# Kernel optimization log

Measured on AMD Instinct MI355X. Metric: run time of the kernel, lower is better.

The kernel has to match this reference:

```python
import math
import jax, jax.numpy as jnp
import numpy as np

DIM = 256
B, S = 4, 4096

def setup_inputs() -> dict:
    key = jax.random.key(0)
    k1, k2, k3 = jax.random.split(key, 3)
    X = jax.random.normal(k1, (B, S, DIM), dtype=jnp.float32)
    # torch nn.Linear(dim, 3*dim): weight [3*dim, dim], bias [3*dim]
    bound = 1.0 / math.sqrt(DIM)
    W = jax.random.uniform(k2, (3 * DIM, DIM), minval=-bound, maxval=bound, dtype=jnp.float32)
    b = jax.random.uniform(k3, (3 * DIM,), minval=-bound, maxval=bound, dtype=jnp.float32)
    return {"X": X, "W": W, "b": b}

def reference(X, W, b):
    # fused QKV projection: X @ W^T + b -> [B, S, 3*dim]
    QKV = jnp.einsum('bsd,ed->bse', X, W) + b
    Q, K, V = jnp.split(QKV, 3, axis=-1)
    # scaled dot-product attention (naive, full score matrix per original)
    scores = jnp.einsum('bqd,bkd->bqk', Q, K) / math.sqrt(DIM)
    att = jax.nn.softmax(scores, axis=-1)
    return jnp.einsum('bqk,bkd->bqd', att, V)
```

## Files before the change

### kernel.cpp

```cpp
#include <hip/hip_runtime.h>
#include <hip/hip_bf16.h>

#define B_ 4
#define S_ 4096
#define D_ 256

typedef __attribute__((ext_vector_type(8))) short bf16x8;
typedef __attribute__((ext_vector_type(4))) short short4v;
typedef __attribute__((ext_vector_type(4))) float f32x4;

static __device__ __forceinline__ unsigned short f2bf(float f) {
    unsigned int u = __float_as_uint(f);
    u += 0x7fffu + ((u >> 16) & 1u);
    return (unsigned short)(u >> 16);
}
static __device__ __forceinline__ float bf2f(unsigned short h) {
    return __uint_as_float(((unsigned int)h) << 16);
}
static __device__ __forceinline__ unsigned int cvtpk(float lo, float hi) {
    unsigned int r;
    asm("v_cvt_pk_bf16_f32 %0, %1, %2" : "=v"(r) : "v"(lo), "v"(hi));
    return r;
}

static __device__ __forceinline__ void gload16(const void* g, void* l) {
    __builtin_amdgcn_global_load_lds(
        (const __attribute__((address_space(1))) unsigned int*)g,
        (__attribute__((address_space(3))) unsigned int*)l, 16, 0, 0);
}

__global__ __launch_bounds__(256) void qkv_proj(
    const float* __restrict__ X, const float* __restrict__ W,
    const float* __restrict__ bias,
    unsigned short* __restrict__ Qb, unsigned short* __restrict__ Kb,
    unsigned short* __restrict__ Vt)
{
    __shared__ __align__(16) unsigned short As[64 * 64];
    __shared__ __align__(16) unsigned short Bs[64 * 64];

    const int tid  = threadIdx.x;
    const int lane = tid & 63;
    const int wid  = tid >> 6;
    const int wm   = wid >> 1, wn = wid & 1;
    const int c    = lane & 15, q4 = lane >> 4;
    const int gm0  = blockIdx.x * 64;
    const int gn0  = blockIdx.y * 64;
    const int sr   = tid >> 2;
    const int sc   = (tid & 3) * 16;

    f32x4 acc[2][2] = {};

    for (int kt = 0; kt < 4; ++kt) {
        const int k0 = kt * 64;
        {
            const float4* ga = (const float4*)(X + (size_t)(gm0 + sr) * D_ + k0 + sc);
            const float4* gb = (const float4*)(W + (size_t)(gn0 + sr) * D_ + k0 + sc);
            float4 a0 = ga[0], a1 = ga[1], a2 = ga[2], a3 = ga[3];
            float4 b0 = gb[0], b1 = gb[1], b2 = gb[2], b3 = gb[3];
            float af[16] = {a0.x,a0.y,a0.z,a0.w, a1.x,a1.y,a1.z,a1.w,
                            a2.x,a2.y,a2.z,a2.w, a3.x,a3.y,a3.z,a3.w};
            float bf[16] = {b0.x,b0.y,b0.z,b0.w, b1.x,b1.y,b1.z,b1.w,
                            b2.x,b2.y,b2.z,b2.w, b3.x,b3.y,b3.z,b3.w};
            bf16x8 av0, av1, bv0, bv1;
            #pragma unroll
            for (int j = 0; j < 8; ++j) {
                av0[j] = (short)f2bf(af[j]);     av1[j] = (short)f2bf(af[8 + j]);
                bv0[j] = (short)f2bf(bf[j]);     bv1[j] = (short)f2bf(bf[8 + j]);
            }
            const int sw = (sr & 7) << 3;
            *(bf16x8*)&As[sr * 64 + ((sc + 0) ^ sw)] = av0;
            *(bf16x8*)&As[sr * 64 + ((sc + 8) ^ sw)] = av1;
            *(bf16x8*)&Bs[sr * 64 + ((sc + 0) ^ sw)] = bv0;
            *(bf16x8*)&Bs[sr * 64 + ((sc + 8) ^ sw)] = bv1;
        }
        __syncthreads();
        const int sw = (c & 7) << 3;
        #pragma unroll
        for (int kk = 0; kk < 64; kk += 32) {
            bf16x8 afr[2], bfr[2];
            #pragma unroll
            for (int mf = 0; mf < 2; ++mf) {
                const int row = wm * 32 + mf * 16 + c;
                afr[mf] = *(const bf16x8*)&As[row * 64 + ((kk + 8 * q4) ^ sw)];
            }
            #pragma unroll
            for (int nf = 0; nf < 2; ++nf) {
                const int row = wn * 32 + nf * 16 + c;
                bfr[nf] = *(const bf16x8*)&Bs[row * 64 + ((kk + 8 * q4) ^ sw)];
            }
            #pragma unroll
            for (int mf = 0; mf < 2; ++mf)
                #pragma unroll
                for (int nf = 0; nf < 2; ++nf)
                    acc[mf][nf] = __builtin_amdgcn_mfma_f32_16x16x32_bf16(
                        afr[mf], bfr[nf], acc[mf][nf], 0, 0, 0);
        }
        __syncthreads();
    }

    const int b  = gm0 >> 12;
    const int s0 = gm0 & 4095;
    #pragma unroll
    for (int mf = 0; mf < 2; ++mf) {
        #pragma unroll
        for (int nf = 0; nf < 2; ++nf) {
            const int e  = gn0 + wn * 32 + nf * 16 + c;
            const float bv = bias[e];
            const int srow0 = s0 + wm * 32 + mf * 16 + 4 * q4;
            if (e < 256) {
                #pragma unroll
                for (int i = 0; i < 4; ++i)
                    Qb[((size_t)b * S_ + srow0 + i) * D_ + e] =
                        f2bf(acc[mf][nf][i] + bv);
            } else if (e < 512) {
                #pragma unroll
                for (int i = 0; i < 4; ++i)
                    Kb[((size_t)b * S_ + srow0 + i) * D_ + (e - 256)] =
                        f2bf(acc[mf][nf][i] + bv);
            } else {
                short4v pv;
                #pragma unroll
                for (int i = 0; i < 4; ++i)
                    pv[i] = (short)f2bf(acc[mf][nf][i] + bv);
                *(short4v*)&Vt[((size_t)(b * D_ + (e - 512))) * S_ + srow0] = pv;
            }
        }
    }
}

__global__ __launch_bounds__(512, 2) void attn_fwd(
    const unsigned short* __restrict__ Qb, const unsigned short* __restrict__ Kb,
    const unsigned short* __restrict__ Vt, float* __restrict__ Out)
{
    __shared__ __align__(16) char smem[132096];

    const int bid  = blockIdx.x;
    const int xcd  = bid & 7;
    const int tile = (xcd >> 1) * 64 + (bid >> 3) * 2 + (xcd & 1);
    const int gr0  = tile * 64;
    const int b    = gr0 >> 12;

    const int tid  = threadIdx.x;
    const int wid  = tid >> 6, lane = tid & 63;
    const int qi   = lane & 15, g = lane >> 4;
    const int rg   = wid & 3;
    const int kh   = wid >> 2;
    const int q0   = gr0 + rg * 16;
    const float C  = 0.09016844005556021f;
    const float THR = 40.0f;

    bf16x8 qf[8];
    {
        const size_t qrow = (size_t)(q0 + qi) * D_ + 8 * g;
        #pragma unroll
        for (int m = 0; m < 8; ++m)
            qf[m] = *(const bf16x8*)&Qb[qrow + m * 32];
    }

    const unsigned short* Kbb = Kb + (size_t)b * S_ * D_;
    const unsigned short* Vtb = Vt + (size_t)b * D_ * S_;

    const int isK = (wid < 4);
    const int sth = (wid >> 1) & 1;
    const int sub = wid & 1;
    int soff[8];
    int doff[8];
    if (isK) {
        const int l5 = lane >> 5, i5 = lane & 31;
        #pragma unroll
        for (int j = 0; j < 8; ++j) {
            const int r0 = sub * 16 + 2 * j + l5;
            soff[j] = (sth * 2048 + r0) * 256 + ((i5 ^ r0) << 3);
            doff[j] = sth * 16384 + (sub * 16 + 2 * j) * 512;
        }
    } else {
        #pragma unroll
        for (int j = 0; j < 8; ++j) {
            const int d = sub * 128 + 16 * j + (lane >> 2);
            soff[j] = d * S_ + sth * 2048 + ((((lane & 3) ^ ((lane >> 3) & 3))) << 3);
            doff[j] = 32768 + sth * 16384 + (sub * 128 + 16 * j) * 64;
        }
    }
    const unsigned short* sbase = isK ? Kbb : Vtb;

    float* Mbuf = (float*)(smem + 131072);
    float* Lbuf = (float*)(smem + 131584);

    f32x4 o[16] = {};
    float m0 = -1.0e30f, l0 = 0.0f;

    #pragma unroll
    for (int j = 0; j < 8; ++j)
        gload16(sbase + soff[j], smem + doff[j]);
    __builtin_amdgcn_s_waitcnt(0);
    __syncthreads();

    const int NS = 64;
    int p = 0;
    const int vsw = (g ^ ((qi >> 1) & 3)) << 4;

    for (int s = 0; s < NS; ++s) {
        if (s + 1 < NS) {
            const unsigned short* sb = sbase + (isK ? (s + 1) * 32 * 256
                                                    : (s + 1) * 32);
            const int bufo = (p ^ 1) * 65536;
            #pragma unroll
            for (int j = 0; j < 8; ++j)
                gload16(sb + soff[j], smem + bufo + doff[j]);
        }

        const char* Ksb = smem + p * 65536 + kh * 16384;
        const char* Vsb = smem + p * 65536 + 32768 + kh * 16384;

        f32x4 sacc[2] = {};
        __builtin_amdgcn_s_setprio(1);
        #pragma unroll
        for (int kc = 0; kc < 2; ++kc) {
            const int kr = kc * 16 + qi;
            const char* krow = Ksb + kr * 512;
            #pragma unroll
            for (int m = 0; m < 8; ++m) {
                bf16x8 kf = *(const bf16x8*)(krow + (((4 * m + g) ^ kr) << 4));
                sacc[kc] = __builtin_amdgcn_mfma_f32_16x16x32_bf16(
                    kf, qf[m], sacc[kc], 0, 0, 0);
            }
        }
        __builtin_amdgcn_s_setprio(0);

        float rmax = fmaxf(fmaxf(fmaxf(sacc[0][0], sacc[0][1]),
                                 fmaxf(sacc[0][2], sacc[0][3])),
                           fmaxf(fmaxf(sacc[1][0], sacc[1][1]),
                                 fmaxf(sacc[1][2], sacc[1][3])));
        rmax = fmaxf(rmax, __shfl_xor(rmax, 16));
        rmax = fmaxf(rmax, __shfl_xor(rmax, 32));

        if (__any(rmax > m0 + THR)) {
            const float mn = fmaxf(m0, rmax);
            const float corr = exp2f((m0 - mn) * C);
            m0 = mn;
            l0 *= corr;
            #pragma unroll
            for (int dc = 0; dc < 16; ++dc)
                #pragma unroll
                for (int r = 0; r < 4; ++r) o[dc][r] *= corr;
        }

        float p8[2][4];
        float rsum = 0.f;
        #pragma unroll
        for (int kc = 0; kc < 2; ++kc)
            #pragma unroll
            for (int r = 0; r < 4; ++r) {
                p8[kc][r] = exp2f((sacc[kc][r] - m0) * C);
                rsum += p8[kc][r];
            }
        rsum += __shfl_xor(rsum, 16);
        rsum += __shfl_xor(rsum, 32);
        l0 += rsum;

        unsigned int pk0[2], pk1[2];
        pk0[0] = cvtpk(p8[0][0], p8[0][1]);  pk0[1] = cvtpk(p8[0][2], p8[0][3]);
        pk1[0] = cvtpk(p8[1][0], p8[1][1]);  pk1[1] = cvtpk(p8[1][2], p8[1][3]);

        const int A0 = qi + ((g & 1) << 5);
        const int A1 = A0 + 16;
        const unsigned int s00 = __shfl(pk0[0], A0), s01 = __shfl(pk0[1], A0);
        const unsigned int s02 = __shfl(pk0[0], A1), s03 = __shfl(pk0[1], A1);
        const unsigned int s10 = __shfl(pk1[0], A0), s11 = __shfl(pk1[1], A0);
        const unsigned int s12 = __shfl(pk1[0], A1), s13 = __shfl(pk1[1], A1);
        const bool hk = (g >> 1);
        union U { unsigned int w[4]; bf16x8 v; } pa;
        pa.w[0] = hk ? s10 : s00;  pa.w[1] = hk ? s11 : s01;
        pa.w[2] = hk ? s12 : s02;  pa.w[3] = hk ? s13 : s03;

        __builtin_amdgcn_s_setprio(1);
        #pragma unroll
        for (int dc = 0; dc < 16; ++dc) {
            bf16x8 vf = *(const bf16x8*)(Vsb + (dc * 16 + qi) * 64 + vsw);
            o[dc] = __builtin_amdgcn_mfma_f32_16x16x32_bf16(vf, pa.v, o[dc], 0, 0, 0);
        }
        __builtin_amdgcn_s_setprio(0);

        __syncthreads();
        p ^= 1;
    }

    const int qidx = rg * 16 + qi;
    if (g == 0) Mbuf[qidx * 2 + kh] = m0;
    __syncthreads();

    {
        const float gm = fmaxf(Mbuf[qidx * 2], Mbuf[qidx * 2 + 1]);
        const float corr = exp2f((m0 - gm) * C);
        l0 *= corr;
        #pragma unroll
        for (int dc = 0; dc < 16; ++dc)
            #pragma unroll
            for (int r = 0; r < 4; ++r) o[dc][r] *= corr;
    }
    if (g == 0) Lbuf[qidx * 2 + kh] = l0;

    float* Obuf = (float*)smem;
    if (kh == 1) {
        #pragma unroll
        for (int dc = 0; dc < 16; ++dc)
            #pragma unroll
            for (int r = 0; r < 4; ++r)
                Obuf[qidx * 260 + dc * 16 + 4 * g + r] = o[dc][r];
    }
    __syncthreads();

    if (kh == 0) {
        const float inv = 1.0f / (Lbuf[qidx * 2] + Lbuf[qidx * 2 + 1]);
        #pragma unroll
        for (int dc = 0; dc < 16; ++dc)
            #pragma unroll
            for (int r = 0; r < 4; ++r) {
                const int d = dc * 16 + 4 * g + r;
                Out[(size_t)(q0 + qi) * D_ + d] =
                    (o[dc][r] + Obuf[qidx * 260 + d]) * inv;
            }
    }
}

extern "C" void kernel_launch(void* const* d_in, const int* in_sizes, int n_in,
                              void* d_out, int out_size, void* d_ws, size_t ws_size,
                              hipStream_t stream) {
    (void)out_size; (void)ws_size;
    const void *Xp = nullptr, *Wp = nullptr, *bp = nullptr;
    for (int i = 0; i < n_in; ++i) {
        if      (in_sizes[i] == B_ * S_ * D_) Xp = d_in[i];
        else if (in_sizes[i] == 3 * D_ * D_)  Wp = d_in[i];
        else if (in_sizes[i] == 3 * D_)       bp = d_in[i];
    }
    if (!Xp) Xp = d_in[0];
    if (!Wp) Wp = d_in[1];
    if (!bp) bp = d_in[2];

    float* Out = (float*)d_out;

    unsigned short* Qb = (unsigned short*)d_ws;
    unsigned short* Kb = Qb + (size_t)B_ * S_ * D_;
    unsigned short* Vt = Kb + (size_t)B_ * S_ * D_;

    dim3 pgrid(256, 12);
    qkv_proj<<<pgrid, 256, 0, stream>>>((const float*)Xp, (const float*)Wp,
                                        (const float*)bp, Qb, Kb, Vt);
    attn_fwd<<<256, 512, 0, stream>>>(Qb, Kb, Vt, Out);
}
```

Before: 158.1 us.

## Shrink KV tile to 16 keys with a 4-stage async LDS pipeline

Halves the key tile per iteration from 32 to 16 rows and replaces the double-buffered loop with a four-buffer ring, issuing loads three tiles ahead and waiting on partial vmcnt before each barrier. The PV product switches to 16x16x16 MFMA, so each lane's P fragment comes straight from its own score accumulators and the cross-lane shuffles are gone. The V tile layout drops its XOR swizzle. This aims to hide global-load latency and remove shuffle overhead, at the cost of twice as many iterations and barriers, smaller MFMAs, and possible LDS bank conflicts on V reads.

```diff
diff --git a/kernel.cpp b/kernel.cpp
--- a/kernel.cpp
+++ b/kernel.cpp
@@ -27,6 +27,29 @@
     __builtin_amdgcn_global_load_lds(
         (const __attribute__((address_space(1))) unsigned int*)g,
         (__attribute__((address_space(3))) unsigned int*)l, 16, 0, 0);
+}
+
+#if __has_builtin(__builtin_amdgcn_mfma_f32_16x16x16bf16_1k)
+#define MFMA16(a, b, c) __builtin_amdgcn_mfma_f32_16x16x16bf16_1k(a, b, c, 0, 0, 0)
+#elif __has_builtin(__builtin_amdgcn_mfma_f32_16x16x16_bf16)
+#define MFMA16(a, b, c) __builtin_amdgcn_mfma_f32_16x16x16_bf16(a, b, c, 0, 0, 0)
+#else
+static __device__ __forceinline__ f32x4 mfma16_asm(short4v a, short4v b, f32x4 c) {
+    asm volatile("v_mfma_f32_16x16x16_bf16 %0, %1, %2, %0"
+                 : "+v"(c) : "v"(a), "v"(b));
+    return c;
+}
+#define MFMA16(a, b, c) mfma16_asm(a, b, c)
+#endif
+
+template<int VW>
+static __device__ __forceinline__ void wait_barrier() {
+    if constexpr (VW == 8)      asm volatile("s_waitcnt vmcnt(8)" ::: "memory");
+    else if constexpr (VW == 4) asm volatile("s_waitcnt vmcnt(4)" ::: "memory");
+    else                        asm volatile("s_waitcnt vmcnt(0)" ::: "memory");
+    __builtin_amdgcn_sched_barrier(0);
+    __builtin_amdgcn_s_barrier();
+    __builtin_amdgcn_sched_barrier(0);
 }
 
 __global__ __launch_bounds__(256) void qkv_proj(
@@ -163,25 +186,24 @@
     const int isK = (wid < 4);
     const int sth = (wid >> 1) & 1;
     const int sub = wid & 1;
-    int soff[8];
-    int doff[8];
+    int soff[4], doff[4];
     if (isK) {
-        const int l5 = lane >> 5, i5 = lane & 31;
-        #pragma unroll
-        for (int j = 0; j < 8; ++j) {
-            const int r0 = sub * 16 + 2 * j + l5;
-            soff[j] = (sth * 2048 + r0) * 256 + ((i5 ^ r0) << 3);
-            doff[j] = sth * 16384 + (sub * 16 + 2 * j) * 512;
+        #pragma unroll
+        for (int j = 0; j < 4; ++j) {
+            const int r0 = sub * 8 + 2 * j + (lane >> 5);
+            soff[j] = (sth * 2048 + r0) * 256 + (((lane & 31) ^ r0) << 3);
+            doff[j] = sth * 8192 + (sub * 8 + 2 * j) * 512;
         }
     } else {
         #pragma unroll
-        for (int j = 0; j < 8; ++j) {
-            const int d = sub * 128 + 16 * j + (lane >> 2);
-            soff[j] = d * S_ + sth * 2048 + ((((lane & 3) ^ ((lane >> 3) & 3))) << 3);
-            doff[j] = 32768 + sth * 16384 + (sub * 128 + 16 * j) * 64;
+        for (int j = 0; j < 4; ++j) {
+            const int d = sub * 128 + 32 * j + (lane >> 1);
+            soff[j] = d * S_ + sth * 2048 + ((lane & 1) << 3);
+            doff[j] = 16384 + sth * 8192 + (sub * 128 + 32 * j) * 32;
         }
     }
     const unsigned short* sbase = isK ? Kbb : Vtb;
+    const int sstride = isK ? 16 * 256 : 16;
 
     float* Mbuf = (float*)(smem + 131072);
     float* Lbuf = (float*)(smem + 131584);
@@ -189,48 +211,37 @@
     f32x4 o[16] = {};
     float m0 = -1.0e30f, l0 = 0.0f;
 
-    #pragma unroll
-    for (int j = 0; j < 8; ++j)
-        gload16(sbase + soff[j], smem + doff[j]);
-    __builtin_amdgcn_s_waitcnt(0);
-    __syncthreads();
-
-    const int NS = 64;
-    int p = 0;
-    const int vsw = (g ^ ((qi >> 1) & 3)) << 4;
-
-    for (int s = 0; s < NS; ++s) {
-        if (s + 1 < NS) {
-            const unsigned short* sb = sbase + (isK ? (s + 1) * 32 * 256
-                                                    : (s + 1) * 32);
-            const int bufo = (p ^ 1) * 65536;
-            #pragma unroll
-            for (int j = 0; j < 8; ++j)
-                gload16(sb + soff[j], smem + bufo + doff[j]);
-        }
-
-        const char* Ksb = smem + p * 65536 + kh * 16384;
-        const char* Vsb = smem + p * 65536 + 32768 + kh * 16384;
-
-        f32x4 sacc[2] = {};
+    auto ISSUE = [&](int t) {
+        char* bb = smem + (size_t)(t & 3) * 32768;
+        const unsigned short* sp = sbase + (size_t)t * sstride;
+        #pragma unroll
+        for (int j = 0; j < 4; ++j)
+            gload16(sp + soff[j], bb + doff[j]);
+    };
+
+    auto COMPUTE = [&](int s) {
+        const char* bb  = smem + (size_t)(s & 3) * 32768;
+        const char* Ksb = bb + kh * 8192;
+        const char* Vsb = bb + 16384 + kh * 8192;
+
+        f32x4 sa = {}, sb2 = {};
         __builtin_amdgcn_s_setprio(1);
         #pragma unroll
-        for (int kc = 0; kc < 2; ++kc) {
-            const int kr = kc * 16 + qi;
-            const char* krow = Ksb + kr * 512;
-            #pragma unroll
-            for (int m = 0; m < 8; ++m) {
-                bf16x8 kf = *(const bf16x8*)(krow + (((4 * m + g) ^ kr) << 4));
-                sacc[kc] = __builtin_amdgcn_mfma_f32_16x16x32_bf16(
-                    kf, qf[m], sacc[kc], 0, 0, 0);
-            }
+        for (int m = 0; m < 4; ++m) {
+            bf16x8 kf = *(const bf16x8*)(Ksb + qi * 512 + (((4 * m + g) ^ qi) << 4));
+            sa = __builtin_amdgcn_mfma_f32_16x16x32_bf16(kf, qf[m], sa, 0, 0, 0);
+        }
+        #pragma unroll
+        for (int m = 4; m < 8; ++m) {
+            bf16x8 kf = *(const bf16x8*)(Ksb + qi * 512 + (((4 * m + g) ^ qi) << 4));
+            sb2 = __builtin_amdgcn_mfma_f32_16x16x32_bf16(kf, qf[m], sb2, 0, 0, 0);
         }
         __builtin_amdgcn_s_setprio(0);
-
-        float rmax = fmaxf(fmaxf(fmaxf(sacc[0][0], sacc[0][1]),
-                                 fmaxf(sacc[0][2], sacc[0][3])),
-                           fmaxf(fmaxf(sacc[1][0], sacc[1][1]),
-                                 fmaxf(sacc[1][2], sacc[1][3])));
+        f32x4 sc;
+        #pragma unroll
+        for (int r = 0; r < 4; ++r) sc[r] = sa[r] + sb2[r];
+
+        float rmax = fmaxf(fmaxf(sc[0], sc[1]), fmaxf(sc[2], sc[3]));
         rmax = fmaxf(rmax, __shfl_xor(rmax, 16));
         rmax = fmaxf(rmax, __shfl_xor(rmax, 32));
 
@@ -245,45 +256,47 @@
                 for (int r = 0; r < 4; ++r) o[dc][r] *= corr;
         }
 
-        float p8[2][4];
+        float p8[4];
         float rsum = 0.f;
         #pragma unroll
-        for (int kc = 0; kc < 2; ++kc)
-            #pragma unroll
-            for (int r = 0; r < 4; ++r) {
-                p8[kc][r] = exp2f((sacc[kc][r] - m0) * C);
-                rsum += p8[kc][r];
-            }
+        for (int r = 0; r < 4; ++r) {
+            p8[r] = exp2f((sc[r] - m0) * C);
+            rsum += p8[r];
+        }
         rsum += __shfl_xor(rsum, 16);
         rsum += __shfl_xor(rsum, 32);
         l0 += rsum;
 
-        unsigned int pk0[2], pk1[2];
-        pk0[0] = cvtpk(p8[0][0], p8[0][1]);  pk0[1] = cvtpk(p8[0][2], p8[0][3]);
-        pk1[0] = cvtpk(p8[1][0], p8[1][1]);  pk1[1] = cvtpk(p8[1][2], p8[1][3]);
-
-        const int A0 = qi + ((g & 1) << 5);
-        const int A1 = A0 + 16;
-        const unsigned int s00 = __shfl(pk0[0], A0), s01 = __shfl(pk0[1], A0);
-        const unsigned int s02 = __shfl(pk0[0], A1), s03 = __shfl(pk0[1], A1);
-        const unsigned int s10 = __shfl(pk1[0], A0), s11 = __shfl(pk1[1], A0);
-        const unsigned int s12 = __shfl(pk1[0], A1), s13 = __shfl(pk1[1], A1);
-        const bool hk = (g >> 1);
-        union U { unsigned int w[4]; bf16x8 v; } pa;
-        pa.w[0] = hk ? s10 : s00;  pa.w[1] = hk ? s11 : s01;
-        pa.w[2] = hk ? s12 : s02;  pa.w[3] = hk ? s13 : s03;
+        union U { unsigned int w[2]; short4v v; } u;
+        u.w[0] = cvtpk(p8[0], p8[1]);
+        u.w[1] = cvtpk(p8[2], p8[3]);
 
         __builtin_amdgcn_s_setprio(1);
         #pragma unroll
         for (int dc = 0; dc < 16; ++dc) {
-            bf16x8 vf = *(const bf16x8*)(Vsb + (dc * 16 + qi) * 64 + vsw);
-            o[dc] = __builtin_amdgcn_mfma_f32_16x16x32_bf16(vf, pa.v, o[dc], 0, 0, 0);
+            short4v vf = *(const short4v*)(Vsb + (dc * 16 + qi) * 32 + g * 8);
+            o[dc] = MFMA16(vf, u.v, o[dc]);
         }
         __builtin_amdgcn_s_setprio(0);
-
-        __syncthreads();
-        p ^= 1;
-    }
+    };
+
+    ISSUE(0); ISSUE(1); ISSUE(2);
+    asm volatile("s_waitcnt vmcnt(8)" ::: "memory");
+    __builtin_amdgcn_sched_barrier(0);
+    __builtin_amdgcn_s_barrier();
+    __builtin_amdgcn_sched_barrier(0);
+
+    const int NS = 128;
+    int s = 0;
+    for (; s < NS - 3; ++s) {
+        ISSUE(s + 3);
+        COMPUTE(s);
+        wait_barrier<8>();
+    }
+    COMPUTE(s); wait_barrier<4>(); ++s;
+    COMPUTE(s); wait_barrier<0>(); ++s;
+    COMPUTE(s);
+    __syncthreads();
 
     const int qidx = rg * 16 + qi;
     if (g == 0) Mbuf[qidx * 2 + kh] = m0;
```

New measurement: 236.4 us. 1.5x slower.
